# Optimization experiments

Hardware: AMD Instinct MI355X
Metric: run time of the kernel (lower is better)

Reference implementation:

```python
import jax, jax.numpy as jnp
import numpy as np

B, S, D, H = 16, 2048, 128, 4
HD = D // H  # 32
EPS = 1e-5


def layer_norm(x, g, b):
    m = jnp.mean(x, axis=-1, keepdims=True)
    v = jnp.mean((x - m) ** 2, axis=-1, keepdims=True)
    return (x - m) * jax.lax.rsqrt(v + EPS) * g + b


def setup_inputs() -> dict:
    key = jax.random.key(0)
    ks = jax.random.split(key, 9)
    lin = lambda k: jax.random.normal(k, (D, D), dtype=jnp.float32) * 0.01  # [in, out]
    return {
        "input0": jax.random.normal(ks[0], (B, S, D), dtype=jnp.float32),
        "Wq": lin(ks[1]), "bq": jnp.zeros((D,), jnp.float32),
        "Wk": lin(ks[2]), "bk": jnp.zeros((D,), jnp.float32),
        "Wv": lin(ks[3]), "bv": jnp.zeros((D,), jnp.float32),
        "Wo": lin(ks[4]), "bo": jnp.zeros((D,), jnp.float32),
        "g1": jnp.ones((D,), jnp.float32), "b1": jnp.zeros((D,), jnp.float32),
        "W1": lin(ks[5]), "bf1": jnp.zeros((D,), jnp.float32),
        "W2": lin(ks[6]), "bf2": jnp.zeros((D,), jnp.float32),
        "g2": jnp.ones((D,), jnp.float32), "b2": jnp.zeros((D,), jnp.float32),
    }


def reference(input0, Wq, bq, Wk, bk, Wv, bv, Wo, bo, g1, b1, W1, bf1, W2, bf2, g2, b2):
    x = input0
    # multi-head attention (self-attention), dropout in eval mode (identity)
    q = (x @ Wq + bq).reshape(B, S, H, HD)
    k = (x @ Wk + bk).reshape(B, S, H, HD)
    v = (x @ Wv + bv).reshape(B, S, H, HD)
    scores = jnp.einsum("bqhd,bkhd->bhqk", q, k) / jnp.sqrt(jnp.float32(HD))
    weights = jax.nn.softmax(scores, axis=-1)
    attn = jnp.einsum("bhqk,bkhd->bqhd", weights, v).reshape(B, S, D)
    attn = attn @ Wo + bo
    attended = layer_norm(attn + x, g1, b1)
    # feed-forward; note residual uses x (not attended), faithful to source
    ff = jax.nn.relu(attended @ W1 + bf1) @ W2 + bf2
    return layer_norm(ff + x, g2, b2)
```

## Files before the change

### kernel.cpp

```cpp
#include <hip/hip_runtime.h>
#include <math.h>

#define NB   16
#define NS   2048
#define ND   128
#define NH   4
#define NHD  32
#define NROWS (NB * NS)

typedef unsigned short u16;
typedef __bf16 bf16x8 __attribute__((ext_vector_type(8)));
typedef float  f32x4  __attribute__((ext_vector_type(4)));
typedef float  f32x16 __attribute__((ext_vector_type(16)));

static __device__ __forceinline__ u16 f2bf(float a) {
    union { __bf16 h; u16 u; } t; t.h = (__bf16)a; return t.u;
}
static __device__ __forceinline__ unsigned int pk2(float a, float b) {
    union { __bf16 h[2]; unsigned int u; } t;
    t.h[0] = (__bf16)a; t.h[1] = (__bf16)b; return t.u;
}

#if __has_builtin(__builtin_amdgcn_exp2f)
#define EXP2(x) __builtin_amdgcn_exp2f(x)
#else
extern "C" __device__ float __ocml_native_exp2_f32(float);
#define EXP2(x) __ocml_native_exp2_f32(x)
#endif

#define QSCALE (0.17677669529663687f * 1.4426950408889634f)

__global__ __launch_bounds__(256) void prep_kernel(
    const float* __restrict__ Wq, const float* __restrict__ Wk,
    const float* __restrict__ Wv, const float* __restrict__ Wo,
    const float* __restrict__ W1, const float* __restrict__ W2,
    u16* __restrict__ wt)
{
    const int wb = blockIdx.x, tid = threadIdx.x;
    const int widx = wb >> 3, sub = wb & 7;
    const float* W = widx == 0 ? Wq : widx == 1 ? Wk : widx == 2 ? Wv
                   : widx == 3 ? Wo : widx == 4 ? W1 : W2;
    const int flat8 = sub * 256 + tid;
    const int n = flat8 >> 4, k0 = (flat8 & 15) * 8;
    float v[8];
    #pragma unroll
    for (int j = 0; j < 8; ++j) v[j] = W[(size_t)(k0 + j) * ND + n];
    int4 o;
    o.x = pk2(v[0], v[1]); o.y = pk2(v[2], v[3]);
    o.z = pk2(v[4], v[5]); o.w = pk2(v[6], v[7]);
    *reinterpret_cast<int4*>(wt + (size_t)widx * 16384 + (size_t)n * ND + k0) = o;
}

__global__ __launch_bounds__(256) void qkv_mfma_kernel(
    const float* __restrict__ x,
    const u16* __restrict__ wtq, const u16* __restrict__ wtk, const u16* __restrict__ wtv,
    const float* __restrict__ bq, const float* __restrict__ bk, const float* __restrict__ bv,
    u16* __restrict__ qo, u16* __restrict__ kvf)
{
    __shared__ __align__(16) u16 tileQ[32][136];
    __shared__ __align__(16) u16 tileK[32][136];

    const int tid = threadIdx.x, lane = tid & 63, w = tid >> 6;
    const int rw = w >> 1, cw = w & 1;
    const int n = lane & 15, c = lane >> 4;
    const int row0 = blockIdx.x * 32;
    const int grow = row0 + rw * 16;

    bf16x8 a[4];
    #pragma unroll
    for (int kk = 0; kk < 4; ++kk) {
        const float* xp = x + (size_t)(grow + n) * ND + kk * 32 + c * 8;
        float4 f0 = *reinterpret_cast<const float4*>(xp);
        float4 f1 = *reinterpret_cast<const float4*>(xp + 4);
        union { unsigned int u[4]; bf16x8 v; } t;
        t.u[0] = pk2(f0.x, f0.y); t.u[1] = pk2(f0.z, f0.w);
        t.u[2] = pk2(f1.x, f1.y); t.u[3] = pk2(f1.z, f1.w);
        a[kk] = t.v;
    }

    f32x4 accq[4], acck[4], accv[4];
    #pragma unroll
    for (int nb = 0; nb < 4; ++nb) {
        accq[nb] = f32x4{0.f, 0.f, 0.f, 0.f};
        acck[nb] = f32x4{0.f, 0.f, 0.f, 0.f};
        accv[nb] = f32x4{0.f, 0.f, 0.f, 0.f};
    }

    #pragma unroll
    for (int kk = 0; kk < 4; ++kk) {
        #pragma unroll
        for (int nb = 0; nb < 4; ++nb) {
            const size_t boff = (size_t)(cw * 64 + nb * 16 + n) * ND + kk * 32 + c * 8;
            bf16x8 bqf = *reinterpret_cast<const bf16x8*>(wtq + boff);
            bf16x8 bkf = *reinterpret_cast<const bf16x8*>(wtk + boff);
            bf16x8 bvf = *reinterpret_cast<const bf16x8*>(wtv + boff);
            accq[nb] = __builtin_amdgcn_mfma_f32_16x16x32_bf16(a[kk], bqf, accq[nb], 0, 0, 0);
            acck[nb] = __builtin_amdgcn_mfma_f32_16x16x32_bf16(a[kk], bkf, acck[nb], 0, 0, 0);
            accv[nb] = __builtin_amdgcn_mfma_f32_16x16x32_bf16(a[kk], bvf, accv[nb], 0, 0, 0);
        }
    }

    const int b    = row0 >> 11;
    const int sp0b = row0 & (NS - 1);
    const int sp0  = sp0b + rw * 16;

    #pragma unroll
    for (int nb = 0; nb < 4; ++nb) {
        const int col = cw * 64 + nb * 16 + n, hh = col >> 5, d32 = col & 31;
        const float bqv = bq[col], bkv = bk[col], bvv = bv[col];

        #pragma unroll
        for (int r = 0; r < 4; ++r) {
            tileQ[rw * 16 + 4 * c + r][col] = f2bf((accq[nb][r] + bqv) * QSCALE);
            tileK[rw * 16 + 4 * c + r][col] = f2bf(acck[nb][r] + bkv);
        }

        const size_t kvb2 = ((size_t)b * NH + hh) * (2 * NS * NHD);
        const int u2    = sp0 >> 4;
        const int lanep = d32 + 32 * (c & 1);
        const int j0    = 4 * (c >> 1);
        float v0 = accv[nb][0] + bvv, v1 = accv[nb][1] + bvv;
        float v2 = accv[nb][2] + bvv, v3 = accv[nb][3] + bvv;
        *reinterpret_cast<uint2*>(
            kvf + kvb2 + (size_t)(u2 >> 1) * 2048 + 1024 + (u2 & 1) * 512
                + (size_t)lanep * 8 + j0) =
            make_uint2(pk2(v0, v1), pk2(v2, v3));
    }

    __syncthreads();

    #pragma unroll
    for (int i = 0; i < 2; ++i) {
        const int flat = tid + i * 256;
        const int lk = flat >> 4, m16 = flat & 15;
        const int col0 = m16 * 8;
        const int hh = col0 >> 5, d32 = col0 & 31;
        const int s2 = d32 >> 4, c22 = (d32 >> 3) & 1;
        const int gk = sp0b + lk;
        const int T = gk >> 5, l5 = gk & 31;
        const size_t kvb  = ((size_t)b * NH + hh) * (NS * NHD);
        const size_t kvb2 = ((size_t)b * NH + hh) * (2 * NS * NHD);
        int4 qv = *reinterpret_cast<const int4*>(&tileQ[lk][col0]);
        *reinterpret_cast<int4*>(qo + kvb + (size_t)gk * NHD + d32) = qv;
        int4 kv = *reinterpret_cast<const int4*>(&tileK[lk][col0]);
        *reinterpret_cast<int4*>(
            kvf + kvb2 + (size_t)T * 2048 + s2 * 512 + (size_t)(l5 + 32 * c22) * 8) = kv;
    }
}

__global__ __launch_bounds__(256) void attn_mfma_kernel(
    const u16* __restrict__ qg,
    const u16* __restrict__ kvf,
    u16* __restrict__ ao)
{
    const int tid = threadIdx.x, lane = tid & 63, w = tid >> 6;

    const int bid  = blockIdx.x;
    const int bh   = (bid & 7) * 8 + ((bid >> 3) & 7);
    const int qblk = bid >> 6;
    const int b = bh >> 2, h = bh & 3;
    const int n = lane & 31, hf = lane >> 5;
    const int q0w = qblk * 128 + w * 32;

    const size_t qbase = (size_t)bh * (NS * NHD);
    const bf16x8 qf0 = *reinterpret_cast<const bf16x8*>(
        qg + qbase + (size_t)(q0w + n) * NHD + 8 * hf);
    const bf16x8 qf1 = *reinterpret_cast<const bf16x8*>(
        qg + qbase + (size_t)(q0w + n) * NHD + 16 + 8 * hf);

    f32x16 ot, zz;
    #pragma unroll
    for (int i = 0; i < 16; ++i) { ot[i] = 0.f; zz[i] = 0.f; }
    float lp0 = 0.f, lp1 = 0.f;

    const u16* kv = kvf + (size_t)bh * (2 * NS * NHD) + (size_t)lane * 8;

    auto EXPPACK = [&](const f32x16& s, bf16x8& w0, bf16x8& w1) {
        union { unsigned int u[4]; bf16x8 v; } a0, a1;
        #pragma unroll
        for (int i = 0; i < 4; ++i) {
            float p0 = EXP2(s[2 * i]), p1 = EXP2(s[2 * i + 1]);
            lp0 += p0; lp1 += p1;
            a0.u[i] = pk2(p0, p1);
        }
        #pragma unroll
        for (int i = 0; i < 4; ++i) {
            float p0 = EXP2(s[8 + 2 * i]), p1 = EXP2(s[9 + 2 * i]);
            lp0 += p0; lp1 += p1;
            a1.u[i] = pk2(p0, p1);
        }
        w0 = a0.v; w1 = a1.v;
    };

    bf16x8 ka0 = *reinterpret_cast<const bf16x8*>(kv);
    bf16x8 ka1 = *reinterpret_cast<const bf16x8*>(kv + 512);
    bf16x8 va0 = *reinterpret_cast<const bf16x8*>(kv + 1024);
    bf16x8 va1 = *reinterpret_cast<const bf16x8*>(kv + 1536);

    for (int t = 0; t < 64; ++t) {
        kv += 2048;

        __builtin_amdgcn_s_setprio(1);
        f32x16 s = __builtin_amdgcn_mfma_f32_32x32x16_bf16(ka0, qf0, zz, 0, 0, 0);
        s = __builtin_amdgcn_mfma_f32_32x32x16_bf16(ka1, qf1, s, 0, 0, 0);
        __builtin_amdgcn_s_setprio(0);

        bf16x8 nka0 = *reinterpret_cast<const bf16x8*>(kv);
        bf16x8 nka1 = *reinterpret_cast<const bf16x8*>(kv + 512);

        bf16x8 pw0, pw1;
        EXPPACK(s, pw0, pw1);

        __builtin_amdgcn_s_setprio(1);
        ot = __builtin_amdgcn_mfma_f32_32x32x16_bf16(va0, pw0, ot, 0, 0, 0);
        ot = __builtin_amdgcn_mfma_f32_32x32x16_bf16(va1, pw1, ot, 0, 0, 0);
        __builtin_amdgcn_s_setprio(0);

        va0 = *reinterpret_cast<const bf16x8*>(kv + 1024);
        va1 = *reinterpret_cast<const bf16x8*>(kv + 1536);
        ka0 = nka0; ka1 = nka1;
    }

    float lp  = lp0 + lp1;
    const float dn  = lp + __shfl_xor(lp, 32);
    const float inv = 1.0f / dn;

    u16* orow = ao + ((size_t)b * NS + q0w + n) * ND + h * NHD + 4 * hf;
    #pragma unroll
    for (int g = 0; g < 4; ++g) {
        uint2 wv = make_uint2(pk2(ot[4 * g] * inv, ot[4 * g + 1] * inv),
                              pk2(ot[4 * g + 2] * inv, ot[4 * g + 3] * inv));
        *reinterpret_cast<uint2*>(orow + 8 * g) = wv;
    }
}

__global__ __launch_bounds__(256) void tail_kernel(
    const u16* __restrict__ A0, const u16* __restrict__ wto,
    const u16* __restrict__ wt1, const u16* __restrict__ wt2,
    const float* __restrict__ bo, const float* __restrict__ bf1,
    const float* __restrict__ bf2, const float* __restrict__ x,
    const float* __restrict__ g1, const float* __restrict__ b1,
    const float* __restrict__ g2, const float* __restrict__ b2,
    float* __restrict__ outp)
{
    __shared__ __align__(16) u16 tile[32][136];
    __shared__ float Sl[2][2][16];
    __shared__ float Sq[2][2][16];

    const int tid = threadIdx.x, lane = tid & 63, w = tid >> 6;
    const int rw = w >> 1, cw = w & 1;
    const int n = lane & 15, c = lane >> 4;
    const int row0 = blockIdx.x * 32;
    const int grow = row0 + rw * 16;
    const int lrow = rw * 16;

    bf16x8 a[4];
    f32x4 acc[4];

    float xres[4][4];
    #pragma unroll
    for (int nb = 0; nb < 4; ++nb) {
        const int col = cw * 64 + nb * 16 + n;
        #pragma unroll
        for (int r = 0; r < 4; ++r)
            xres[nb][r] = x[(size_t)(grow + 4 * c + r) * ND + col];
    }

    #pragma unroll
    for (int kk = 0; kk < 4; ++kk)
        a[kk] = *reinterpret_cast<const bf16x8*>(
            A0 + (size_t)(grow + n) * ND + kk * 32 + c * 8);
    #pragma unroll
    for (int nb = 0; nb < 4; ++nb) acc[nb] = f32x4{0.f, 0.f, 0.f, 0.f};
    #pragma unroll
    for (int kk = 0; kk < 4; ++kk)
        #pragma unroll
        for (int nb = 0; nb < 4; ++nb) {
            bf16x8 bw = *reinterpret_cast<const bf16x8*>(
                wto + (size_t)(cw * 64 + nb * 16 + n) * ND + kk * 32 + c * 8);
            acc[nb] = __builtin_amdgcn_mfma_f32_16x16x32_bf16(a[kk], bw, acc[nb], 0, 0, 0);
        }

    {
        float vals[4][4];
        float sr[4]  = {0.f, 0.f, 0.f, 0.f};
        float sr2[4] = {0.f, 0.f, 0.f, 0.f};
        #pragma unroll
        for (int nb = 0; nb < 4; ++nb) {
            const float bb = bo[cw * 64 + nb * 16 + n];
            #pragma unroll
            for (int r = 0; r < 4; ++r) {
                float vv = acc[nb][r] + bb + xres[nb][r];
                vals[nb][r] = vv;
                sr[r]  += vv;
                sr2[r] += vv * vv;
            }
        }
        #pragma unroll
        for (int m = 1; m < 16; m <<= 1)
            #pragma unroll
            for (int r = 0; r < 4; ++r) {
                sr[r]  += __shfl_xor(sr[r],  m);
                sr2[r] += __shfl_xor(sr2[r], m);
            }
        if (n == 0) {
            #pragma unroll
            for (int r = 0; r < 4; ++r) {
                Sl[rw][cw][4 * c + r] = sr[r];
                Sq[rw][cw][4 * c + r] = sr2[r];
            }
        }
        __syncthreads();
        #pragma unroll
        for (int r = 0; r < 4; ++r) {
            float st  = Sl[rw][0][4 * c + r] + Sl[rw][1][4 * c + r];
            float st2 = Sq[rw][0][4 * c + r] + Sq[rw][1][4 * c + r];
            float mean = st * (1.f / 128.f);
            float var  = fmaf(-mean, mean, st2 * (1.f / 128.f));
            float rstd = rsqrtf(var + 1e-5f);
            #pragma unroll
            for (int nb = 0; nb < 4; ++nb) {
                const int col = cw * 64 + nb * 16 + n;
                float y = fmaf((vals[nb][r] - mean) * rstd, g1[col], b1[col]);
                tile[lrow + 4 * c + r][col] = f2bf(y);
            }
        }
    }
    __syncthreads();

    #pragma unroll
    for (int kk = 0; kk < 4; ++kk)
        a[kk] = *reinterpret_cast<const bf16x8*>(&tile[lrow + n][kk * 32 + c * 8]);
    __syncthreads();
    #pragma unroll
    for (int nb = 0; nb < 4; ++nb) acc[nb] = f32x4{0.f, 0.f, 0.f, 0.f};
    #pragma unroll
    for (int kk = 0; kk < 4; ++kk)
        #pragma unroll
        for (int nb = 0; nb < 4; ++nb) {
            bf16x8 bw = *reinterpret_cast<const bf16x8*>(
                wt1 + (size_t)(cw * 64 + nb * 16 + n) * ND + kk * 32 + c * 8);
            acc[nb] = __builtin_amdgcn_mfma_f32_16x16x32_bf16(a[kk], bw, acc[nb], 0, 0, 0);
        }
    #pragma unroll
    for (int nb = 0; nb < 4; ++nb) {
        const int col = cw * 64 + nb * 16 + n;
        const float bb = bf1[col];
        #pragma unroll
        for (int r = 0; r < 4; ++r)
            tile[lrow + 4 * c + r][col] = f2bf(fmaxf(acc[nb][r] + bb, 0.f));
    }
    __syncthreads();

    #pragma unroll
    for (int kk = 0; kk < 4; ++kk)
        a[kk] = *reinterpret_cast<const bf16x8*>(&tile[lrow + n][kk * 32 + c * 8]);
    #pragma unroll
    for (int nb = 0; nb < 4; ++nb) acc[nb] = f32x4{0.f, 0.f, 0.f, 0.f};
    #pragma unroll
    for (int kk = 0; kk < 4; ++kk)
        #pragma unroll
        for (int nb = 0; nb < 4; ++nb) {
            bf16x8 bw = *reinterpret_cast<const bf16x8*>(
                wt2 + (size_t)(cw * 64 + nb * 16 + n) * ND + kk * 32 + c * 8);
            acc[nb] = __builtin_amdgcn_mfma_f32_16x16x32_bf16(a[kk], bw, acc[nb], 0, 0, 0);
        }
    {
        float vals[4][4];
        float sr[4]  = {0.f, 0.f, 0.f, 0.f};
        float sr2[4] = {0.f, 0.f, 0.f, 0.f};
        #pragma unroll
        for (int nb = 0; nb < 4; ++nb) {
            const float bb = bf2[cw * 64 + nb * 16 + n];
            #pragma unroll
            for (int r = 0; r < 4; ++r) {
                float vv = acc[nb][r] + bb + xres[nb][r];
                vals[nb][r] = vv;
                sr[r]  += vv;
                sr2[r] += vv * vv;
            }
        }
        #pragma unroll
        for (int m = 1; m < 16; m <<= 1)
            #pragma unroll
            for (int r = 0; r < 4; ++r) {
                sr[r]  += __shfl_xor(sr[r],  m);
                sr2[r] += __shfl_xor(sr2[r], m);
            }
        __syncthreads();
        if (n == 0) {
            #pragma unroll
            for (int r = 0; r < 4; ++r) {
                Sl[rw][cw][4 * c + r] = sr[r];
                Sq[rw][cw][4 * c + r] = sr2[r];
            }
        }
        __syncthreads();
        #pragma unroll
        for (int r = 0; r < 4; ++r) {
            float st  = Sl[rw][0][4 * c + r] + Sl[rw][1][4 * c + r];
            float st2 = Sq[rw][0][4 * c + r] + Sq[rw][1][4 * c + r];
            float mean = st * (1.f / 128.f);
            float var  = fmaf(-mean, mean, st2 * (1.f / 128.f));
            float rstd = rsqrtf(var + 1e-5f);
            #pragma unroll
            for (int nb = 0; nb < 4; ++nb) {
                const int col = cw * 64 + nb * 16 + n;
                float y = fmaf((vals[nb][r] - mean) * rstd, g2[col], b2[col]);
                outp[(size_t)(grow + 4 * c + r) * ND + col] = y;
            }
        }
    }
}

extern "C" void kernel_launch(void* const* d_in, const int* in_sizes, int n_in,
                              void* d_out, int out_size, void* d_ws, size_t ws_size,
                              hipStream_t stream)
{
    const float* x   = (const float*)d_in[0];
    const float* Wq  = (const float*)d_in[1];
    const float* bq  = (const float*)d_in[2];
    const float* Wk  = (const float*)d_in[3];
    const float* bk  = (const float*)d_in[4];
    const float* Wv  = (const float*)d_in[5];
    const float* bv  = (const float*)d_in[6];
    const float* Wo  = (const float*)d_in[7];
    const float* bo  = (const float*)d_in[8];
    const float* g1  = (const float*)d_in[9];
    const float* b1  = (const float*)d_in[10];
    const float* W1  = (const float*)d_in[11];
    const float* bf1 = (const float*)d_in[12];
    const float* W2  = (const float*)d_in[13];
    const float* bf2 = (const float*)d_in[14];
    const float* g2  = (const float*)d_in[15];
    const float* b2  = (const float*)d_in[16];
    float* outp = (float*)d_out;

    const size_t NE = (size_t)NROWS * ND;
    u16* wt  = (u16*)d_ws;
    u16* qb  = wt + 6 * 16384;
    u16* kvb = qb + NE;
    u16* aob = kvb + 2 * NE;

    prep_kernel<<<dim3(48), dim3(256), 0, stream>>>(Wq, Wk, Wv, Wo, W1, W2, wt);
    qkv_mfma_kernel<<<dim3(NROWS / 32), dim3(256), 0, stream>>>(
        x, wt + 0 * 16384, wt + 1 * 16384, wt + 2 * 16384, bq, bk, bv, qb, kvb);
    attn_mfma_kernel<<<dim3(1024), dim3(256), 0, stream>>>(qb, kvb, aob);
    tail_kernel<<<dim3(NROWS / 32), dim3(256), 0, stream>>>(
        aob, wt + 3 * 16384, wt + 4 * 16384, wt + 5 * 16384,
        bo, bf1, bf2, x, g1, b1, g2, b2, outp);
}
```

Before: 135.7 us.

## Split attention keys across wave pairs, compute denominators via MFMA, drop QKV LDS staging

The attention kernel now gives each 32-query group to two waves, each covering half the key range. Their partial outputs and denominators are merged through shared memory, and the grid doubles to 2048 blocks for more parallelism. The softmax denominator is now an MFMA against a ones vector instead of scalar adds. The loop is software-pipelined two tiles deep, so the score MFMA of one tile overlaps the PV MFMA of the previous one. The QKV kernel swaps operand order for Q/K so results land directly in the target layout, which removes the LDS tile staging and the barrier, at the cost of narrower 8-byte scattered global stores.

```diff
diff --git a/kernel.cpp b/kernel.cpp
--- a/kernel.cpp
+++ b/kernel.cpp
@@ -57,9 +57,6 @@
     const float* __restrict__ bq, const float* __restrict__ bk, const float* __restrict__ bv,
     u16* __restrict__ qo, u16* __restrict__ kvf)
 {
-    __shared__ __align__(16) u16 tileQ[32][136];
-    __shared__ __align__(16) u16 tileK[32][136];
-
     const int tid = threadIdx.x, lane = tid & 63, w = tid >> 6;
     const int rw = w >> 1, cw = w & 1;
     const int n = lane & 15, c = lane >> 4;
@@ -94,57 +91,51 @@
             bf16x8 bqf = *reinterpret_cast<const bf16x8*>(wtq + boff);
             bf16x8 bkf = *reinterpret_cast<const bf16x8*>(wtk + boff);
             bf16x8 bvf = *reinterpret_cast<const bf16x8*>(wtv + boff);
-            accq[nb] = __builtin_amdgcn_mfma_f32_16x16x32_bf16(a[kk], bqf, accq[nb], 0, 0, 0);
-            acck[nb] = __builtin_amdgcn_mfma_f32_16x16x32_bf16(a[kk], bkf, acck[nb], 0, 0, 0);
+            accq[nb] = __builtin_amdgcn_mfma_f32_16x16x32_bf16(bqf, a[kk], accq[nb], 0, 0, 0);
+            acck[nb] = __builtin_amdgcn_mfma_f32_16x16x32_bf16(bkf, a[kk], acck[nb], 0, 0, 0);
             accv[nb] = __builtin_amdgcn_mfma_f32_16x16x32_bf16(a[kk], bvf, accv[nb], 0, 0, 0);
         }
     }
 
-    const int b    = row0 >> 11;
-    const int sp0b = row0 & (NS - 1);
-    const int sp0  = sp0b + rw * 16;
+    const int b   = row0 >> 11;
+    const int sp0 = (row0 & (NS - 1)) + rw * 16;
+    const int spos = sp0 + n;
+    const int T = spos >> 5, l5 = spos & 31;
 
     #pragma unroll
     for (int nb = 0; nb < 4; ++nb) {
-        const int col = cw * 64 + nb * 16 + n, hh = col >> 5, d32 = col & 31;
-        const float bqv = bq[col], bkv = bk[col], bvv = bv[col];
-
-        #pragma unroll
-        for (int r = 0; r < 4; ++r) {
-            tileQ[rw * 16 + 4 * c + r][col] = f2bf((accq[nb][r] + bqv) * QSCALE);
-            tileK[rw * 16 + 4 * c + r][col] = f2bf(acck[nb][r] + bkv);
-        }
-
+        const int d0  = cw * 64 + nb * 16 + 4 * c;
+        const int hh  = d0 >> 5, d32 = d0 & 31;
+        const size_t kvb  = ((size_t)b * NH + hh) * (NS * NHD);
         const size_t kvb2 = ((size_t)b * NH + hh) * (2 * NS * NHD);
-        const int u2    = sp0 >> 4;
-        const int lanep = d32 + 32 * (c & 1);
-        const int j0    = 4 * (c >> 1);
+        const float4 bq4 = *reinterpret_cast<const float4*>(bq + d0);
+        const float4 bk4 = *reinterpret_cast<const float4*>(bk + d0);
+        float q0 = (accq[nb][0] + bq4.x) * QSCALE;
+        float q1 = (accq[nb][1] + bq4.y) * QSCALE;
+        float q2 = (accq[nb][2] + bq4.z) * QSCALE;
+        float q3 = (accq[nb][3] + bq4.w) * QSCALE;
+        *reinterpret_cast<uint2*>(qo + kvb + (size_t)spos * NHD + d32) =
+            make_uint2(pk2(q0, q1), pk2(q2, q3));
+        float k0 = acck[nb][0] + bk4.x, k1 = acck[nb][1] + bk4.y;
+        float k2 = acck[nb][2] + bk4.z, k3 = acck[nb][3] + bk4.w;
+        const int s2 = d32 >> 4, c2 = (d32 >> 3) & 1, j0 = d32 & 7;
+        *reinterpret_cast<uint2*>(
+            kvf + kvb2 + (size_t)T * 2048 + s2 * 512 + (size_t)(l5 + 32 * c2) * 8 + j0) =
+            make_uint2(pk2(k0, k1), pk2(k2, k3));
+
+        const int dcol = cw * 64 + nb * 16 + n;
+        const int hhv = dcol >> 5, dv32 = dcol & 31;
+        const size_t kvb2v = ((size_t)b * NH + hhv) * (2 * NS * NHD);
+        const float bvv = bv[dcol];
+        const int u2 = sp0 >> 4;
+        const int lanep = dv32 + 32 * (c & 1);
+        const int jv0 = 4 * (c >> 1);
         float v0 = accv[nb][0] + bvv, v1 = accv[nb][1] + bvv;
         float v2 = accv[nb][2] + bvv, v3 = accv[nb][3] + bvv;
         *reinterpret_cast<uint2*>(
-            kvf + kvb2 + (size_t)(u2 >> 1) * 2048 + 1024 + (u2 & 1) * 512
-                + (size_t)lanep * 8 + j0) =
+            kvf + kvb2v + (size_t)(u2 >> 1) * 2048 + 1024 + (u2 & 1) * 512
+                + (size_t)lanep * 8 + jv0) =
             make_uint2(pk2(v0, v1), pk2(v2, v3));
-    }
-
-    __syncthreads();
-
-    #pragma unroll
-    for (int i = 0; i < 2; ++i) {
-        const int flat = tid + i * 256;
-        const int lk = flat >> 4, m16 = flat & 15;
-        const int col0 = m16 * 8;
-        const int hh = col0 >> 5, d32 = col0 & 31;
-        const int s2 = d32 >> 4, c22 = (d32 >> 3) & 1;
-        const int gk = sp0b + lk;
-        const int T = gk >> 5, l5 = gk & 31;
-        const size_t kvb  = ((size_t)b * NH + hh) * (NS * NHD);
-        const size_t kvb2 = ((size_t)b * NH + hh) * (2 * NS * NHD);
-        int4 qv = *reinterpret_cast<const int4*>(&tileQ[lk][col0]);
-        *reinterpret_cast<int4*>(qo + kvb + (size_t)gk * NHD + d32) = qv;
-        int4 kv = *reinterpret_cast<const int4*>(&tileK[lk][col0]);
-        *reinterpret_cast<int4*>(
-            kvf + kvb2 + (size_t)T * 2048 + s2 * 512 + (size_t)(l5 + 32 * c22) * 8) = kv;
     }
 }
 
@@ -153,14 +144,18 @@
     const u16* __restrict__ kvf,
     u16* __restrict__ ao)
 {
+    __shared__ float Ol[2][64][17];
+    __shared__ float Dl[2][64];
+
     const int tid = threadIdx.x, lane = tid & 63, w = tid >> 6;
+    const int qhalf = w >> 1, khalf = w & 1;
 
     const int bid  = blockIdx.x;
     const int bh   = (bid & 7) * 8 + ((bid >> 3) & 7);
     const int qblk = bid >> 6;
     const int b = bh >> 2, h = bh & 3;
     const int n = lane & 31, hf = lane >> 5;
-    const int q0w = qblk * 128 + w * 32;
+    const int q0w = qblk * 64 + qhalf * 32;
 
     const size_t qbase = (size_t)bh * (NS * NHD);
     const bf16x8 qf0 = *reinterpret_cast<const bf16x8*>(
@@ -168,69 +163,110 @@
     const bf16x8 qf1 = *reinterpret_cast<const bf16x8*>(
         qg + qbase + (size_t)(q0w + n) * NHD + 16 + 8 * hf);
 
-    f32x16 ot, zz;
-    #pragma unroll
-    for (int i = 0; i < 16; ++i) { ot[i] = 0.f; zz[i] = 0.f; }
-    float lp0 = 0.f, lp1 = 0.f;
-
-    const u16* kv = kvf + (size_t)bh * (2 * NS * NHD) + (size_t)lane * 8;
-
+    union { unsigned int u[4]; bf16x8 v; } ONES;
+    ONES.u[0] = 0x3F803F80u; ONES.u[1] = 0x3F803F80u;
+    ONES.u[2] = 0x3F803F80u; ONES.u[3] = 0x3F803F80u;
+
+    f32x16 ot, dn, zz;
+    #pragma unroll
+    for (int i = 0; i < 16; ++i) { ot[i] = 0.f; dn[i] = 0.f; zz[i] = 0.f; }
+
+    const u16* kv = kvf + (size_t)bh * (2 * NS * NHD) + (size_t)lane * 8
+                        + (size_t)khalf * 32 * 2048;
+
+    auto LDK = [&](int t, int half) {
+        return *reinterpret_cast<const bf16x8*>(kv + (size_t)t * 2048 + half * 512);
+    };
+    auto LDV = [&](int t, int half) {
+        return *reinterpret_cast<const bf16x8*>(kv + (size_t)t * 2048 + 1024 + half * 512);
+    };
     auto EXPPACK = [&](const f32x16& s, bf16x8& w0, bf16x8& w1) {
         union { unsigned int u[4]; bf16x8 v; } a0, a1;
         #pragma unroll
-        for (int i = 0; i < 4; ++i) {
-            float p0 = EXP2(s[2 * i]), p1 = EXP2(s[2 * i + 1]);
-            lp0 += p0; lp1 += p1;
-            a0.u[i] = pk2(p0, p1);
-        }
-        #pragma unroll
-        for (int i = 0; i < 4; ++i) {
-            float p0 = EXP2(s[8 + 2 * i]), p1 = EXP2(s[9 + 2 * i]);
-            lp0 += p0; lp1 += p1;
-            a1.u[i] = pk2(p0, p1);
-        }
+        for (int i = 0; i < 4; ++i)
+            a0.u[i] = pk2(EXP2(s[2 * i]), EXP2(s[2 * i + 1]));
+        #pragma unroll
+        for (int i = 0; i < 4; ++i)
+            a1.u[i] = pk2(EXP2(s[8 + 2 * i]), EXP2(s[9 + 2 * i]));
         w0 = a0.v; w1 = a1.v;
     };
 
-    bf16x8 ka0 = *reinterpret_cast<const bf16x8*>(kv);
-    bf16x8 ka1 = *reinterpret_cast<const bf16x8*>(kv + 512);
-    bf16x8 va0 = *reinterpret_cast<const bf16x8*>(kv + 1024);
-    bf16x8 va1 = *reinterpret_cast<const bf16x8*>(kv + 1536);
-
-    for (int t = 0; t < 64; ++t) {
-        kv += 2048;
-
+    bf16x8 kA0 = LDK(0, 0), kA1 = LDK(0, 1);
+    bf16x8 vA0 = LDV(0, 0), vA1 = LDV(0, 1);
+    f32x16 s;
+    s = __builtin_amdgcn_mfma_f32_32x32x16_bf16(kA0, qf0, zz, 0, 0, 0);
+    s = __builtin_amdgcn_mfma_f32_32x32x16_bf16(kA1, qf1, s, 0, 0, 0);
+    bf16x8 kB0 = LDK(1, 0), kB1 = LDK(1, 1);
+    bf16x8 pA0, pA1;
+    EXPPACK(s, pA0, pA1);
+
+    for (int j = 0; j < 15; ++j) {
+        const int t = 2 * j;
+        bf16x8 vB0 = LDV(t + 1, 0), vB1 = LDV(t + 1, 1);
+        bf16x8 nk0 = LDK(t + 2, 0), nk1 = LDK(t + 2, 1);
         __builtin_amdgcn_s_setprio(1);
-        f32x16 s = __builtin_amdgcn_mfma_f32_32x32x16_bf16(ka0, qf0, zz, 0, 0, 0);
-        s = __builtin_amdgcn_mfma_f32_32x32x16_bf16(ka1, qf1, s, 0, 0, 0);
+        s  = __builtin_amdgcn_mfma_f32_32x32x16_bf16(kB0, qf0, zz, 0, 0, 0);
+        s  = __builtin_amdgcn_mfma_f32_32x32x16_bf16(kB1, qf1, s, 0, 0, 0);
+        ot = __builtin_amdgcn_mfma_f32_32x32x16_bf16(vA0, pA0, ot, 0, 0, 0);
+        dn = __builtin_amdgcn_mfma_f32_32x32x16_bf16(ONES.v, pA0, dn, 0, 0, 0);
+        ot = __builtin_amdgcn_mfma_f32_32x32x16_bf16(vA1, pA1, ot, 0, 0, 0);
+        dn = __builtin_amdgcn_mfma_f32_32x32x16_bf16(ONES.v, pA1, dn, 0, 0, 0);
         __builtin_amdgcn_s_setprio(0);
-
-        bf16x8 nka0 = *reinterpret_cast<const bf16x8*>(kv);
-        bf16x8 nka1 = *reinterpret_cast<const bf16x8*>(kv + 512);
-
-        bf16x8 pw0, pw1;
-        EXPPACK(s, pw0, pw1);
-
+        bf16x8 pB0, pB1;
+        EXPPACK(s, pB0, pB1);
+
+        vA0 = LDV(t + 2, 0); vA1 = LDV(t + 2, 1);
+        kB0 = LDK(t + 3, 0); kB1 = LDK(t + 3, 1);
         __builtin_amdgcn_s_setprio(1);
-        ot = __builtin_amdgcn_mfma_f32_32x32x16_bf16(va0, pw0, ot, 0, 0, 0);
-        ot = __builtin_amdgcn_mfma_f32_32x32x16_bf16(va1, pw1, ot, 0, 0, 0);
+        s  = __builtin_amdgcn_mfma_f32_32x32x16_bf16(nk0, qf0, zz, 0, 0, 0);
+        s  = __builtin_amdgcn_mfma_f32_32x32x16_bf16(nk1, qf1, s, 0, 0, 0);
+        ot = __builtin_amdgcn_mfma_f32_32x32x16_bf16(vB0, pB0, ot, 0, 0, 0);
+        dn = __builtin_amdgcn_mfma_f32_32x32x16_bf16(ONES.v, pB0, dn, 0, 0, 0);
+        ot = __builtin_amdgcn_mfma_f32_32x32x16_bf16(vB1, pB1, ot, 0, 0, 0);
+        dn = __builtin_amdgcn_mfma_f32_32x32x16_bf16(ONES.v, pB1, dn, 0, 0, 0);
         __builtin_amdgcn_s_setprio(0);
-
-        va0 = *reinterpret_cast<const bf16x8*>(kv + 1024);
-        va1 = *reinterpret_cast<const bf16x8*>(kv + 1536);
-        ka0 = nka0; ka1 = nka1;
-    }
-
-    float lp  = lp0 + lp1;
-    const float dn  = lp + __shfl_xor(lp, 32);
-    const float inv = 1.0f / dn;
-
-    u16* orow = ao + ((size_t)b * NS + q0w + n) * ND + h * NHD + 4 * hf;
-    #pragma unroll
-    for (int g = 0; g < 4; ++g) {
-        uint2 wv = make_uint2(pk2(ot[4 * g] * inv, ot[4 * g + 1] * inv),
-                              pk2(ot[4 * g + 2] * inv, ot[4 * g + 3] * inv));
-        *reinterpret_cast<uint2*>(orow + 8 * g) = wv;
+        EXPPACK(s, pA0, pA1);
+    }
+
+    {
+        bf16x8 vB0 = LDV(31, 0), vB1 = LDV(31, 1);
+        __builtin_amdgcn_s_setprio(1);
+        s  = __builtin_amdgcn_mfma_f32_32x32x16_bf16(kB0, qf0, zz, 0, 0, 0);
+        s  = __builtin_amdgcn_mfma_f32_32x32x16_bf16(kB1, qf1, s, 0, 0, 0);
+        ot = __builtin_amdgcn_mfma_f32_32x32x16_bf16(vA0, pA0, ot, 0, 0, 0);
+        dn = __builtin_amdgcn_mfma_f32_32x32x16_bf16(ONES.v, pA0, dn, 0, 0, 0);
+        ot = __builtin_amdgcn_mfma_f32_32x32x16_bf16(vA1, pA1, ot, 0, 0, 0);
+        dn = __builtin_amdgcn_mfma_f32_32x32x16_bf16(ONES.v, pA1, dn, 0, 0, 0);
+        __builtin_amdgcn_s_setprio(0);
+        bf16x8 pB0, pB1;
+        EXPPACK(s, pB0, pB1);
+        __builtin_amdgcn_s_setprio(1);
+        ot = __builtin_amdgcn_mfma_f32_32x32x16_bf16(vB0, pB0, ot, 0, 0, 0);
+        dn = __builtin_amdgcn_mfma_f32_32x32x16_bf16(ONES.v, pB0, dn, 0, 0, 0);
+        ot = __builtin_amdgcn_mfma_f32_32x32x16_bf16(vB1, pB1, ot, 0, 0, 0);
+        dn = __builtin_amdgcn_mfma_f32_32x32x16_bf16(ONES.v, pB1, dn, 0, 0, 0);
+        __builtin_amdgcn_s_setprio(0);
+    }
+
+    if (khalf) {
+        #pragma unroll
+        for (int i = 0; i < 16; ++i) Ol[qhalf][lane][i] = ot[i];
+        Dl[qhalf][lane] = dn[0];
+    }
+    __syncthreads();
+    if (!khalf) {
+        #pragma unroll
+        for (int i = 0; i < 16; ++i) ot[i] += Ol[qhalf][lane][i];
+        const float dnt = dn[0] + Dl[qhalf][lane];
+        const float inv = 1.0f / dnt;
+
+        u16* orow = ao + ((size_t)b * NS + q0w + n) * ND + h * NHD + 4 * hf;
+        #pragma unroll
+        for (int g = 0; g < 4; ++g) {
+            uint2 wv = make_uint2(pk2(ot[4 * g] * inv, ot[4 * g + 1] * inv),
+                                  pk2(ot[4 * g + 2] * inv, ot[4 * g + 3] * inv));
+            *reinterpret_cast<uint2*>(orow + 8 * g) = wv;
+        }
     }
 }
 
@@ -445,7 +481,7 @@
     prep_kernel<<<dim3(48), dim3(256), 0, stream>>>(Wq, Wk, Wv, Wo, W1, W2, wt);
     qkv_mfma_kernel<<<dim3(NROWS / 32), dim3(256), 0, stream>>>(
         x, wt + 0 * 16384, wt + 1 * 16384, wt + 2 * 16384, bq, bk, bv, qb, kvb);
-    attn_mfma_kernel<<<dim3(1024), dim3(256), 0, stream>>>(qb, kvb, aob);
+    attn_mfma_kernel<<<dim3(2048), dim3(256), 0, stream>>>(qb, kvb, aob);
     tail_kernel<<<dim3(NROWS / 32), dim3(256), 0, stream>>>(
         aob, wt + 3 * 16384, wt + 4 * 16384, wt + 5 * 16384,
         bo, bf1, bf2, x, g1, b1, g2, b2, outp);
```

Result: faster. 127.6 us (-6.0%).
